# Performance work log

Measured on AMD Instinct MI355X. Metric: run time of the kernel, lower is better.

Reference implementation:

```python
import jax, jax.numpy as jnp
import numpy as np

B, N, F = 8, 512, 128
H, U = 4, 32
LEAKY_ALPHA = 0.2

def setup_inputs() -> dict:
    key = jax.random.key(0)
    k1, k2, k3, k4 = jax.random.split(key, 4)
    inputs = jax.random.normal(k1, (B, N, F), dtype=jnp.float32)
    # glorot-ish scaled params
    W_src = jax.random.normal(k2, (H, F, U), dtype=jnp.float32) * (2.0 / (F + U)) ** 0.5
    W_dst = jax.random.normal(k3, (H, F, U), dtype=jnp.float32) * (2.0 / (F + U)) ** 0.5
    a = jax.random.normal(k4, (H, U, 1), dtype=jnp.float32) * (2.0 / (U + 1)) ** 0.5
    return {"inputs": inputs, "W_src": W_src, "W_dst": W_dst, "a": a}

def reference(inputs, W_src, W_dst, a):
    # GATv2, eval mode (no dropout). Loop over the small fixed head count to
    # keep peak memory at one (B,N,N,U) pairwise tensor at a time, matching
    # the original per-head loop.
    outs = []
    for h in range(W_src.shape[0]):
        h_src = inputs @ W_src[h]          # (B, N, U)
        h_dst = inputs @ W_dst[h]          # (B, N, U)
        # pairwise[b,i,j,:] = h_src[b,i] + h_dst[b,j]
        pair = jax.nn.leaky_relu(h_src[:, :, None, :] + h_dst[:, None, :, :],
                                 negative_slope=LEAKY_ALPHA)  # (B,N,N,U)
        scores = jnp.einsum('biju,u->bij', pair, a[h, :, 0])   # (B,N,N)
        attn = jax.nn.softmax(scores, axis=-1)
        outs.append(attn @ h_src)          # (B,N,U) -- weighted sum of h_src
    return jnp.concatenate(outs, axis=-1)  # concat_heads=True -> (B,N,H*U)
```

## Files before the change

### kernel.cpp

```cpp
#include <hip/hip_runtime.h>
#include <hip/hip_bf16.h>

#define B_ 8
#define N_ 512
#define F_ 128
#define H_ 4
#define U_ 32
#define LEAKY_ALPHA 0.2f
#define PS 520
#define DS 36

typedef __attribute__((ext_vector_type(8))) short short8;
typedef __attribute__((ext_vector_type(4))) float f32x4;

static __device__ __forceinline__ short f2bf_s(float x) {
    __hip_bfloat16 hv = __float2bfloat16(x);
    return *reinterpret_cast<short*>(&hv);
}
static __device__ __forceinline__ float bf2f_s(short v) {
    return __uint_as_float(((unsigned)(unsigned short)v) << 16);
}

__global__ __launch_bounds__(256) void proj_kernel(
    const float* __restrict__ x, const float* __restrict__ Wsrc,
    const float* __restrict__ Wdst, const float* __restrict__ a,
    float* __restrict__ hsrc, float* __restrict__ hdstN,
    float* __restrict__ Drow, float* __restrict__ ascaled,
    short* __restrict__ hsrcT)
{
    __shared__ float4 xlds[8 * 32];
    const int t  = threadIdx.x;
    const int r0 = blockIdx.x * 8;

    const float4* xg = (const float4*)x + (size_t)r0 * 32;
    xlds[t] = xg[t];
    __syncthreads();

    const int u     = t & 31;
    const int h     = (t >> 5) & 3;
    const int which = t >> 7;
    const float* W  = (which ? Wdst : Wsrc) + h * (F_ * U_) + u;

    float acc[8];
#pragma unroll
    for (int r = 0; r < 8; ++r) acc[r] = 0.f;

#pragma unroll 2
    for (int fc = 0; fc < 32; ++fc) {
        const float w0 = W[(4 * fc + 0) * U_];
        const float w1 = W[(4 * fc + 1) * U_];
        const float w2 = W[(4 * fc + 2) * U_];
        const float w3 = W[(4 * fc + 3) * U_];
#pragma unroll
        for (int r = 0; r < 8; ++r) {
            const float4 xv = xlds[r * 32 + fc];
            float s = acc[r];
            s = fmaf(xv.x, w0, s);
            s = fmaf(xv.y, w1, s);
            s = fmaf(xv.z, w2, s);
            s = fmaf(xv.w, w3, s);
            acc[r] = s;
        }
    }

    const float av = a[h * U_ + u];
    if (which == 1 && blockIdx.x == 0)
        ascaled[h * U_ + u] = (1.f - LEAKY_ALPHA) * av;

    const int b  = r0 >> 9;
    const int n0 = r0 & (N_ - 1);

    if (which == 0) {
        short8 pk;
#pragma unroll
        for (int r = 0; r < 8; ++r) {
            const size_t base = ((size_t)((b * H_ + h) * N_ + n0 + r) << 5) + u;
            hsrc[base] = acc[r];
            pk[r] = f2bf_s(acc[r]);
        }
        *(short8*)&hsrcT[((size_t)((b * H_ + h) * U_) + u) * N_ + n0] = pk;
    } else {
#pragma unroll
        for (int r = 0; r < 8; ++r) {
            const size_t base = ((size_t)((b * H_ + h) * N_ + n0 + r) << 5) + u;
            hdstN[base] = -acc[r];
            float v = acc[r] * av;
            v += __shfl_xor(v, 1);
            v += __shfl_xor(v, 2);
            v += __shfl_xor(v, 4);
            v += __shfl_xor(v, 8);
            v += __shfl_xor(v, 16);
            if (u == 0) Drow[(b * H_ + h) * N_ + n0 + r] = v;
        }
    }
}

__global__ __launch_bounds__(256, 4) void attn_kernel(
    const float* __restrict__ hsrc, const float* __restrict__ hdstN,
    const float* __restrict__ Drow, const float* __restrict__ ascaled,
    const short* __restrict__ hsrcT, float* __restrict__ out)
{
    __shared__ float dlds[128 * DS];
    __shared__ __align__(16) short pbf[16 * PS];
    __shared__ f32x4 scr[4][64];
    __shared__ float lfin[16];

    const int t    = threadIdx.x;
    const int L    = t & 63;
    const int w    = __builtin_amdgcn_readfirstlane(t >> 6);
    const int tile = blockIdx.x & 31;
    const int bh   = blockIdx.x >> 5;
    const int h    = bh & 3;
    const int b    = bh >> 2;
    const size_t bhN = (size_t)bh * N_;
    const int ig0  = tile * 16;
    const int i    = t >> 4;
    const int sub  = t & 15;

    float4 s4[8], a4[8];
    {
        const float4* sg = (const float4*)(hsrc + ((bhN + ig0 + i) << 5));
        const float4* ag = (const float4*)(ascaled + h * U_);
#pragma unroll
        for (int q = 0; q < 8; ++q) s4[q] = sg[q];
#pragma unroll
        for (int q = 0; q < 8; ++q) a4[q] = ag[q];
    }

    const float4* dg = (const float4*)(hdstN + (bhN << 5));
    const float* Dr  = Drow + bhN;

    float l = 0.f;

    float4 pre0 = dg[t];
    float4 pre1 = dg[t + 256];
    float4 pre2 = dg[t + 512];
    float4 pre3 = dg[t + 768];

    for (int jt = 0; jt < 4; ++jt) {
        __syncthreads();
        {
            const int i0 = t,       j0 = i0 >> 3, u0 = i0 & 7;
            const int i1 = t + 256, j1 = i1 >> 3, u1 = i1 & 7;
            const int i2 = t + 512, j2 = i2 >> 3, u2 = i2 & 7;
            const int i3 = t + 768, j3 = i3 >> 3, u3 = i3 & 7;
            *(float4*)&dlds[j0 * DS + u0 * 4] = pre0;
            *(float4*)&dlds[j1 * DS + u1 * 4] = pre1;
            *(float4*)&dlds[j2 * DS + u2 * 4] = pre2;
            *(float4*)&dlds[j3 * DS + u3 * 4] = pre3;
        }
        __syncthreads();
        if (jt < 3) {
            const float4* dn = dg + (jt + 1) * 1024;
            pre0 = dn[t];
            pre1 = dn[t + 256];
            pre2 = dn[t + 512];
            pre3 = dn[t + 768];
        }

#pragma unroll
        for (int k = 0; k < 8; ++k) {
            const int jl = sub + 16 * k;
            const float4* dr = (const float4*)&dlds[jl * DS];
            float ra = 0.f, rb = 0.f;
#pragma unroll
            for (int q = 0; q < 8; q += 2) {
                const float4 d0 = dr[q];
                const float4 d1 = dr[q + 1];
                ra = fmaf(a4[q].x, fmaxf(s4[q].x, d0.x), ra);
                rb = fmaf(a4[q].y, fmaxf(s4[q].y, d0.y), rb);
                ra = fmaf(a4[q].z, fmaxf(s4[q].z, d0.z), ra);
                rb = fmaf(a4[q].w, fmaxf(s4[q].w, d0.w), rb);
                ra = fmaf(a4[q + 1].x, fmaxf(s4[q + 1].x, d1.x), ra);
                rb = fmaf(a4[q + 1].y, fmaxf(s4[q + 1].y, d1.y), rb);
                ra = fmaf(a4[q + 1].z, fmaxf(s4[q + 1].z, d1.z), ra);
                rb = fmaf(a4[q + 1].w, fmaxf(s4[q + 1].w, d1.w), rb);
            }
            const float Dj = Dr[jt * 128 + jl];
            const float e  = __expf(Dj + ra + rb);
            const short qv = f2bf_s(e);
            pbf[i * PS + jt * 128 + jl] = qv;
            l += bf2f_s(qv);
        }
    }

    l += __shfl_xor(l, 1);
    l += __shfl_xor(l, 2);
    l += __shfl_xor(l, 4);
    l += __shfl_xor(l, 8);
    if (sub == 0) lfin[i] = __builtin_amdgcn_rcpf(l);
    __syncthreads();

    const int m  = L & 15;
    const int kq = L >> 4;
    const int nt = w & 1;
    const int ks = w >> 1;
    const short* Ap = pbf + m * PS + ks * 256 + kq * 8;
    const short* Bp = hsrcT + ((size_t)bh * U_ + nt * 16 + m) * N_ + ks * 256 + kq * 8;

    f32x4 acc = {0.f, 0.f, 0.f, 0.f};
#pragma unroll
    for (int st = 0; st < 8; ++st) {
        const short8 af = *(const short8*)(Ap + st * 32);
        const short8 bf = *(const short8*)(Bp + st * 32);
        acc = __builtin_amdgcn_mfma_f32_16x16x32_bf16(af, bf, acc, 0, 0, 0);
    }
    scr[w][L] = acc;
    __syncthreads();

    if (w < 2) {
        const f32x4 p0 = scr[w][L];
        const f32x4 p1 = scr[w + 2][L];
#pragma unroll
        for (int r = 0; r < 4; ++r) {
            const int il = kq * 4 + r;
            out[((size_t)(b * N_ + ig0 + il)) * (H_ * U_) + h * U_ + w * 16 + m]
                = (p0[r] + p1[r]) * lfin[il];
        }
    }
}

extern "C" void kernel_launch(void* const* d_in, const int* in_sizes, int n_in,
                              void* d_out, int out_size, void* d_ws, size_t ws_size,
                              hipStream_t stream) {
    const float* x    = (const float*)d_in[0];
    const float* Wsrc = (const float*)d_in[1];
    const float* Wdst = (const float*)d_in[2];
    const float* a    = (const float*)d_in[3];

    float* ws      = (float*)d_ws;
    float* hsrc    = ws;
    float* hdstN   = hsrc + (size_t)B_ * H_ * N_ * U_;
    float* Drow    = hdstN + (size_t)B_ * H_ * N_ * U_;
    float* ascaled = Drow + (size_t)B_ * H_ * N_;
    short* hsrcT   = (short*)(ascaled + H_ * U_);

    proj_kernel<<<(B_ * N_) / 8, 256, 0, stream>>>(x, Wsrc, Wdst, a,
                                                   hsrc, hdstN, Drow, ascaled,
                                                   hsrcT);
    attn_kernel<<<B_ * H_ * (N_ / 16), 256, 0, stream>>>(hsrc, hdstN, Drow,
                                                         ascaled, hsrcT,
                                                         (float*)d_out);
}
```

Before: 99.27 us.

## Remap score loop so each thread owns one key column across eight query rows

```diff
diff --git a/kernel.cpp b/kernel.cpp
--- a/kernel.cpp
+++ b/kernel.cpp
@@ -8,7 +8,7 @@
 #define U_ 32
 #define LEAKY_ALPHA 0.2f
 #define PS 520
-#define DS 36
+#define TS 133
 
 typedef __attribute__((ext_vector_type(8))) short short8;
 typedef __attribute__((ext_vector_type(4))) float f32x4;
@@ -100,37 +100,37 @@
     const float* __restrict__ Drow, const float* __restrict__ ascaled,
     const short* __restrict__ hsrcT, float* __restrict__ out)
 {
-    __shared__ float dlds[128 * DS];
+    __shared__ float dt[32 * TS];
     __shared__ __align__(16) short pbf[16 * PS];
     __shared__ f32x4 scr[4][64];
+    __shared__ float lpart[4][8];
     __shared__ float lfin[16];
 
     const int t    = threadIdx.x;
     const int L    = t & 63;
     const int w    = __builtin_amdgcn_readfirstlane(t >> 6);
+    const int p8   = w >> 1;
+    const int jl   = t & 127;
     const int tile = blockIdx.x & 31;
     const int bh   = blockIdx.x >> 5;
     const int h    = bh & 3;
     const int b    = bh >> 2;
     const size_t bhN = (size_t)bh * N_;
     const int ig0  = tile * 16;
-    const int i    = t >> 4;
-    const int sub  = t & 15;
-
-    float4 s4[8], a4[8];
+
+    float4 av4[8];
     {
-        const float4* sg = (const float4*)(hsrc + ((bhN + ig0 + i) << 5));
         const float4* ag = (const float4*)(ascaled + h * U_);
 #pragma unroll
-        for (int q = 0; q < 8; ++q) s4[q] = sg[q];
-#pragma unroll
-        for (int q = 0; q < 8; ++q) a4[q] = ag[q];
+        for (int q = 0; q < 8; ++q) av4[q] = ag[q];
     }
 
     const float4* dg = (const float4*)(hdstN + (bhN << 5));
-    const float* Dr  = Drow + bhN;
-
-    float l = 0.f;
+    const float* srow_base = hsrc + ((bhN + ig0 + p8 * 8) << 5);
+
+    float lp[8];
+#pragma unroll
+    for (int k = 0; k < 8; ++k) lp[k] = 0.f;
 
     float4 pre0 = dg[t];
     float4 pre1 = dg[t + 256];
@@ -140,14 +140,17 @@
     for (int jt = 0; jt < 4; ++jt) {
         __syncthreads();
         {
-            const int i0 = t,       j0 = i0 >> 3, u0 = i0 & 7;
-            const int i1 = t + 256, j1 = i1 >> 3, u1 = i1 & 7;
-            const int i2 = t + 512, j2 = i2 >> 3, u2 = i2 & 7;
-            const int i3 = t + 768, j3 = i3 >> 3, u3 = i3 & 7;
-            *(float4*)&dlds[j0 * DS + u0 * 4] = pre0;
-            *(float4*)&dlds[j1 * DS + u1 * 4] = pre1;
-            *(float4*)&dlds[j2 * DS + u2 * 4] = pre2;
-            *(float4*)&dlds[j3 * DS + u3 * 4] = pre3;
+#define COMMIT(pre, qq)                                          \
+            {                                                    \
+                const int idx = t + 256 * (qq);                  \
+                const int j = idx >> 3, u4 = idx & 7;            \
+                dt[(4 * u4 + 0) * TS + j] = pre.x;               \
+                dt[(4 * u4 + 1) * TS + j] = pre.y;               \
+                dt[(4 * u4 + 2) * TS + j] = pre.z;               \
+                dt[(4 * u4 + 3) * TS + j] = pre.w;               \
+            }
+            COMMIT(pre0, 0) COMMIT(pre1, 1) COMMIT(pre2, 2) COMMIT(pre3, 3)
+#undef COMMIT
         }
         __syncthreads();
         if (jt < 3) {
@@ -158,38 +161,51 @@
             pre3 = dn[t + 768];
         }
 
-#pragma unroll
-        for (int k = 0; k < 8; ++k) {
-            const int jl = sub + 16 * k;
-            const float4* dr = (const float4*)&dlds[jl * DS];
-            float ra = 0.f, rb = 0.f;
-#pragma unroll
-            for (int q = 0; q < 8; q += 2) {
-                const float4 d0 = dr[q];
-                const float4 d1 = dr[q + 1];
-                ra = fmaf(a4[q].x, fmaxf(s4[q].x, d0.x), ra);
-                rb = fmaf(a4[q].y, fmaxf(s4[q].y, d0.y), rb);
-                ra = fmaf(a4[q].z, fmaxf(s4[q].z, d0.z), ra);
-                rb = fmaf(a4[q].w, fmaxf(s4[q].w, d0.w), rb);
-                ra = fmaf(a4[q + 1].x, fmaxf(s4[q + 1].x, d1.x), ra);
-                rb = fmaf(a4[q + 1].y, fmaxf(s4[q + 1].y, d1.y), rb);
-                ra = fmaf(a4[q + 1].z, fmaxf(s4[q + 1].z, d1.z), ra);
-                rb = fmaf(a4[q + 1].w, fmaxf(s4[q + 1].w, d1.w), rb);
+        float d[32];
+#pragma unroll
+        for (int u = 0; u < 32; ++u) d[u] = dt[u * TS + jl];
+
+        const float Dj = Drow[bhN + jt * 128 + jl];
+
+#pragma unroll
+        for (int ii = 0; ii < 8; ++ii) {
+            const float* srow = srow_base + (ii << 5);
+            float acA = 0.f, acB = 0.f;
+#pragma unroll
+            for (int q = 0; q < 8; ++q) {
+                acA = fmaf(av4[q].x, fmaxf(srow[4 * q + 0], d[4 * q + 0]), acA);
+                acB = fmaf(av4[q].y, fmaxf(srow[4 * q + 1], d[4 * q + 1]), acB);
+                acA = fmaf(av4[q].z, fmaxf(srow[4 * q + 2], d[4 * q + 2]), acA);
+                acB = fmaf(av4[q].w, fmaxf(srow[4 * q + 3], d[4 * q + 3]), acB);
             }
-            const float Dj = Dr[jt * 128 + jl];
-            const float e  = __expf(Dj + ra + rb);
+            const float e  = __expf(Dj + acA + acB);
             const short qv = f2bf_s(e);
-            pbf[i * PS + jt * 128 + jl] = qv;
-            l += bf2f_s(qv);
-        }
-    }
-
-    l += __shfl_xor(l, 1);
-    l += __shfl_xor(l, 2);
-    l += __shfl_xor(l, 4);
-    l += __shfl_xor(l, 8);
-    if (sub == 0) lfin[i] = __builtin_amdgcn_rcpf(l);
+            pbf[(p8 * 8 + ii) * PS + jt * 128 + jl] = qv;
+            lp[ii] += bf2f_s(qv);
+        }
+    }
+
+#pragma unroll
+    for (int k = 0; k < 8; ++k) {
+        float v = lp[k];
+        v += __shfl_xor(v, 1);
+        v += __shfl_xor(v, 2);
+        v += __shfl_xor(v, 4);
+        v += __shfl_xor(v, 8);
+        v += __shfl_xor(v, 16);
+        v += __shfl_xor(v, 32);
+        lp[k] = v;
+    }
+    if (L == 0) {
+#pragma unroll
+        for (int k = 0; k < 8; ++k) lpart[w][k] = lp[k];
+    }
     __syncthreads();
+
+    if (t < 16) {
+        const int ii = t & 7, ph = t >> 3;
+        lfin[t] = __builtin_amdgcn_rcpf(lpart[2 * ph][ii] + lpart[2 * ph + 1][ii]);
+    }
 
     const int m  = L & 15;
     const int kq = L >> 4;
@@ -209,13 +225,13 @@
     __syncthreads();
 
     if (w < 2) {
-        const f32x4 p0 = scr[w][L];
-        const f32x4 p1 = scr[w + 2][L];
+        const f32x4 q0 = scr[w][L];
+        const f32x4 q1 = scr[w + 2][L];
 #pragma unroll
         for (int r = 0; r < 4; ++r) {
             const int il = kq * 4 + r;
             out[((size_t)(b * N_ + ig0 + il)) * (H_ * U_) + h * U_ + w * 16 + m]
-                = (p0[r] + p1[r]) * lfin[il];
+                = (q0[r] + q1[r]) * lfin[il];
         }
     }
 }
```

Measured after the change: 111.8 us. 12.6% more time.
